# Kernel tuning notes

Hardware: AMD Instinct MI355X
Metric: run time of the kernel (lower is better)

## Reference

```python
import jax, jax.numpy as jnp
import numpy as np

BS, LX, LY, H, MD = 16, 1024, 1024, 512, 512


def setup_inputs() -> dict:
    key = jax.random.key(0)
    ks = jax.random.split(key, 8)
    x = jax.random.normal(ks[0], (BS, LX, H), dtype=jnp.float32)
    y = jax.random.normal(ks[1], (BS, LY, H), dtype=jnp.float32)
    y_mask = jax.random.bernoulli(ks[2], 0.2, (BS, LY))  # True = masked
    s1 = 1.0 / np.sqrt(H)
    W1 = jax.random.uniform(ks[3], (MD, H), jnp.float32, -s1, s1)
    b1 = jax.random.uniform(ks[4], (MD,), jnp.float32, -s1, s1)
    W2 = jax.random.uniform(ks[5], (MD, H), jnp.float32, -s1, s1)
    b2 = jax.random.uniform(ks[6], (MD,), jnp.float32, -s1, s1)
    s2 = 1.0 / np.sqrt(MD)
    k7, k8 = jax.random.split(ks[7])
    w_o = jax.random.uniform(k7, (MD,), jnp.float32, -s2, s2)
    b_o = jax.random.uniform(k8, (), jnp.float32, -s2, s2)
    return {"x": x, "y": y, "y_mask": y_mask, "W1": W1, "b1": b1,
            "W2": W2, "b2": b2, "w_o": w_o, "b_o": b_o}


def reference(x, y, y_mask, W1, b1, W2, b2, w_o, b_o):
    # Projections: [B,L,MD]
    x_proj = jax.nn.relu(jnp.einsum('blh,mh->blm', x, W1) + b1)
    y_proj = jax.nn.relu(jnp.einsum('blh,mh->blm', y, W2) + b2)
    # o_liner is linear, so o_liner(x_i + y_j) = w_o.x_i + w_o.y_j + b_o
    sx = x_proj @ w_o  # [B,Lx]
    sy = y_proj @ w_o  # [B,Ly]
    scores = sx[:, :, None] + sy[:, None, :] + b_o  # [B,Lx,Ly]
    scores = jnp.where(y_mask[:, None, :], jnp.float32(-1e7), scores)
    alpha = jax.nn.softmax(scores, axis=-1)  # softmax over len_y
    return alpha
```

## Files before the change

### kernel.cpp

```cpp
#include <hip/hip_runtime.h>
#include <hip/hip_bf16.h>

#define BS 16
#define LX 1024
#define LY 1024
#define H 512
#define MD 512
#define RY (BS * LY)

typedef __attribute__((ext_vector_type(8))) __bf16 bf16x8;
typedef __attribute__((ext_vector_type(4))) float floatx4;

__device__ __forceinline__ void load_lds16(const __bf16* g, __bf16* l) {
    __builtin_amdgcn_global_load_lds(
        (const __attribute__((address_space(1))) void*)g,
        (__attribute__((address_space(3))) void*)l,
        16, 0, 0);
}

__global__ __launch_bounds__(256) void prep(const float* __restrict__ Y,
                                            const float* __restrict__ W2,
                                            __bf16* __restrict__ yb,
                                            __bf16* __restrict__ wb) {
    const long i = (long)blockIdx.x * 256 + threadIdx.x;
    const float* src; __bf16* dst; long off;
    if (blockIdx.x < 4096) { src = Y;  dst = yb; off = i; }
    else                   { src = W2; dst = wb; off = i - 4096L * 256; }
    const float4 a = *(const float4*)(src + off * 8);
    const float4 b = *(const float4*)(src + off * 8 + 4);
    bf16x8 v = { (__bf16)a.x, (__bf16)a.y, (__bf16)a.z, (__bf16)a.w,
                 (__bf16)b.x, (__bf16)b.y, (__bf16)b.z, (__bf16)b.w };
    *(bf16x8*)(dst + off * 8) = v;
}

#define BM 64
#define BN 128
#define BKT 64
__global__ __launch_bounds__(256) void gemm_sy(const __bf16* __restrict__ yb,
                                               const __bf16* __restrict__ wb,
                                               const float* __restrict__ b2,
                                               const float* __restrict__ wo,
                                               float* __restrict__ part) {
    __shared__ __align__(16) __bf16 As[BM * BKT];
    __shared__ __align__(16) __bf16 Bs[BN * BKT];

    const int tid  = threadIdx.x;
    const int lane = tid & 63;
    const int wave = tid >> 6;
    const int wm = wave >> 1;
    const int wn = wave & 1;
    const int la = lane & 15;
    const int qa = lane >> 4;
    const int nt = blockIdx.x;
    const int mt = blockIdx.y;
    const int m0 = mt * BM, n0 = nt * BN;

    const int lrow = lane >> 3;
    const int lcol = (lane & 7) * 8;

    floatx4 acc[2][4] = {};

    for (int k0 = 0; k0 < H; k0 += BKT) {
        __syncthreads();
        #pragma unroll
        for (int r = 0; r < 2; ++r) {
            const int rb = r * 32 + wave * 8;
            load_lds16(yb + (size_t)(m0 + rb + lrow) * H + k0 + lcol, &As[rb * BKT]);
        }
        #pragma unroll
        for (int r = 0; r < 4; ++r) {
            const int rb = r * 32 + wave * 8;
            load_lds16(wb + (size_t)(n0 + rb + lrow) * H + k0 + lcol, &Bs[rb * BKT]);
        }
        __syncthreads();

        #pragma unroll
        for (int kh = 0; kh < 2; ++kh) {
            bf16x8 afr[2], bfr[4];
            #pragma unroll
            for (int mf = 0; mf < 2; ++mf)
                afr[mf] = *(const bf16x8*)&As[(wm * 32 + mf * 16 + la) * BKT + kh * 32 + qa * 8];
            #pragma unroll
            for (int nf = 0; nf < 4; ++nf)
                bfr[nf] = *(const bf16x8*)&Bs[(wn * 64 + nf * 16 + la) * BKT + kh * 32 + qa * 8];
            #pragma unroll
            for (int mf = 0; mf < 2; ++mf)
                #pragma unroll
                for (int nf = 0; nf < 4; ++nf)
                    acc[mf][nf] = __builtin_amdgcn_mfma_f32_16x16x32_bf16(afr[mf], bfr[nf], acc[mf][nf], 0, 0, 0);
        }
    }

    const int slice = nt * 2 + wn;
    #pragma unroll
    for (int mf = 0; mf < 2; ++mf) {
        #pragma unroll
        for (int reg = 0; reg < 4; ++reg) {
            float s = 0.f;
            #pragma unroll
            for (int nf = 0; nf < 4; ++nf) {
                const int n = n0 + wn * 64 + nf * 16 + la;
                float v = acc[mf][nf][reg] + b2[n];
                v = fmaxf(v, 0.f);
                s += v * wo[n];
            }
            s += __shfl_xor(s, 1);
            s += __shfl_xor(s, 2);
            s += __shfl_xor(s, 4);
            s += __shfl_xor(s, 8);
            if (la == 0) {
                const int m = m0 + wm * 32 + mf * 16 + qa * 4 + reg;
                part[(size_t)slice * RY + m] = s;
            }
        }
    }
}

__global__ __launch_bounds__(256) void softmax_p(const float* __restrict__ part,
                                                 const int* __restrict__ mask,
                                                 float* __restrict__ p) {
    const int b = blockIdx.x;
    const int tid = threadIdx.x;
    __shared__ float red[8];

    float vals[4];
    int   ms[4];
    float mx = -INFINITY;
    #pragma unroll
    for (int c = 0; c < 4; ++c) {
        const int j = c * 256 + tid;
        float v = 0.f;
        #pragma unroll
        for (int t = 0; t < 8; ++t) v += part[t * RY + b * LY + j];
        vals[c] = v;
        ms[c]   = mask[b * LY + j];
        if (!ms[c]) mx = fmaxf(mx, v);
    }
    #pragma unroll
    for (int off = 1; off < 64; off <<= 1) mx = fmaxf(mx, __shfl_xor(mx, off));
    if ((tid & 63) == 0) red[tid >> 6] = mx;
    __syncthreads();
    mx = fmaxf(fmaxf(red[0], red[1]), fmaxf(red[2], red[3]));

    float e[4];
    float sum = 0.f;
    #pragma unroll
    for (int c = 0; c < 4; ++c) {
        e[c] = ms[c] ? 0.f : __expf(vals[c] - mx);
        sum += e[c];
    }
    #pragma unroll
    for (int off = 1; off < 64; off <<= 1) sum += __shfl_xor(sum, off);
    if ((tid & 63) == 0) red[4 + (tid >> 6)] = sum;
    __syncthreads();
    sum = red[4] + red[5] + red[6] + red[7];
    const float inv = 1.0f / sum;

    #pragma unroll
    for (int c = 0; c < 4; ++c)
        p[b * LY + c * 256 + tid] = e[c] * inv;
}

__global__ __launch_bounds__(256) void bcast(const float* __restrict__ p,
                                             float4* __restrict__ out) {
    const int tid = threadIdx.x;
    const long base_row = (long)blockIdx.x * 8;
    const int b = (int)(base_row >> 10);
    const float4 v = *(const float4*)(p + b * LY + tid * 4);
    float4* o = out + base_row * (LY / 4) + tid;
    #pragma unroll
    for (int r = 0; r < 8; ++r) o[r * (LY / 4)] = v;
}

extern "C" void kernel_launch(void* const* d_in, const int* in_sizes, int n_in,
                              void* d_out, int out_size, void* d_ws, size_t ws_size,
                              hipStream_t stream) {
    const float* y  = (const float*)d_in[1];
    const int*   ym = (const int*)  d_in[2];
    const float* W2 = (const float*)d_in[5];
    const float* b2 = (const float*)d_in[6];
    const float* wo = (const float*)d_in[7];

    char* ws = (char*)d_ws;
    __bf16* yb   = (__bf16*)ws;
    __bf16* wb   = (__bf16*)(ws + (size_t)RY * H * 2);
    float*  part = (float*)(ws + (size_t)RY * H * 2 + (size_t)MD * H * 2);
    float*  p    = part + 8 * RY;

    prep<<<4096 + 128, 256, 0, stream>>>(y, W2, yb, wb);
    dim3 gg(MD / BN, RY / BM);
    gemm_sy<<<gg, 256, 0, stream>>>(yb, wb, b2, wo, part);
    softmax_p<<<BS, 256, 0, stream>>>(part, ym, p);
    bcast<<<(BS * LX) / 8, 256, 0, stream>>>(p, (float4*)d_out);
}
```

Baseline: 151.9 us.

## Fuse Y fp32-to-bf16 conversion into GEMM A-tile load with padded LDS

Removes the separate conversion pass over Y and instead loads fp32 Y tiles directly in the GEMM, converting to bf16 in registers before storing to LDS with a padded row stride. The intent is to drop the intermediate bf16 Y write and re-read. In exchange, the GEMM reads fp32 Y (twice the bytes per tile, read by each of four column blocks), and the A path loses the async global-to-LDS load.

```diff
diff --git a/kernel.cpp b/kernel.cpp
--- a/kernel.cpp
+++ b/kernel.cpp
@@ -18,30 +18,26 @@
         16, 0, 0);
 }
 
-__global__ __launch_bounds__(256) void prep(const float* __restrict__ Y,
-                                            const float* __restrict__ W2,
-                                            __bf16* __restrict__ yb,
-                                            __bf16* __restrict__ wb) {
-    const long i = (long)blockIdx.x * 256 + threadIdx.x;
-    const float* src; __bf16* dst; long off;
-    if (blockIdx.x < 4096) { src = Y;  dst = yb; off = i; }
-    else                   { src = W2; dst = wb; off = i - 4096L * 256; }
-    const float4 a = *(const float4*)(src + off * 8);
-    const float4 b = *(const float4*)(src + off * 8 + 4);
+__global__ __launch_bounds__(256) void prep_w2(const float* __restrict__ W2,
+                                               __bf16* __restrict__ wb) {
+    const int i = blockIdx.x * 256 + threadIdx.x;
+    const float4 a = *(const float4*)(W2 + (size_t)i * 8);
+    const float4 b = *(const float4*)(W2 + (size_t)i * 8 + 4);
     bf16x8 v = { (__bf16)a.x, (__bf16)a.y, (__bf16)a.z, (__bf16)a.w,
                  (__bf16)b.x, (__bf16)b.y, (__bf16)b.z, (__bf16)b.w };
-    *(bf16x8*)(dst + off * 8) = v;
+    *(bf16x8*)(wb + (size_t)i * 8) = v;
 }
 
 #define BM 64
 #define BN 128
 #define BKT 64
-__global__ __launch_bounds__(256) void gemm_sy(const __bf16* __restrict__ yb,
+#define ASTR 72
+__global__ __launch_bounds__(256) void gemm_sy(const float* __restrict__ Y,
                                                const __bf16* __restrict__ wb,
                                                const float* __restrict__ b2,
                                                const float* __restrict__ wo,
                                                float* __restrict__ part) {
-    __shared__ __align__(16) __bf16 As[BM * BKT];
+    __shared__ __align__(16) __bf16 As[BM * ASTR];
     __shared__ __align__(16) __bf16 Bs[BN * BKT];
 
     const int tid  = threadIdx.x;
@@ -58,20 +54,29 @@
     const int lrow = lane >> 3;
     const int lcol = (lane & 7) * 8;
 
+    const int ar = tid >> 2;
+    const int ac = (tid & 3) * 16;
+    const float* ybase = Y + (size_t)(m0 + ar) * H + ac;
+
     floatx4 acc[2][4] = {};
 
     for (int k0 = 0; k0 < H; k0 += BKT) {
         __syncthreads();
         #pragma unroll
-        for (int r = 0; r < 2; ++r) {
-            const int rb = r * 32 + wave * 8;
-            load_lds16(yb + (size_t)(m0 + rb + lrow) * H + k0 + lcol, &As[rb * BKT]);
-        }
-        #pragma unroll
         for (int r = 0; r < 4; ++r) {
             const int rb = r * 32 + wave * 8;
             load_lds16(wb + (size_t)(n0 + rb + lrow) * H + k0 + lcol, &Bs[rb * BKT]);
         }
+        const float4 a0 = *(const float4*)(ybase + k0);
+        const float4 a1 = *(const float4*)(ybase + k0 + 4);
+        const float4 a2 = *(const float4*)(ybase + k0 + 8);
+        const float4 a3 = *(const float4*)(ybase + k0 + 12);
+        bf16x8 p0 = { (__bf16)a0.x, (__bf16)a0.y, (__bf16)a0.z, (__bf16)a0.w,
+                      (__bf16)a1.x, (__bf16)a1.y, (__bf16)a1.z, (__bf16)a1.w };
+        bf16x8 p1 = { (__bf16)a2.x, (__bf16)a2.y, (__bf16)a2.z, (__bf16)a2.w,
+                      (__bf16)a3.x, (__bf16)a3.y, (__bf16)a3.z, (__bf16)a3.w };
+        *(bf16x8*)&As[ar * ASTR + ac]     = p0;
+        *(bf16x8*)&As[ar * ASTR + ac + 8] = p1;
         __syncthreads();
 
         #pragma unroll
@@ -79,7 +84,7 @@
             bf16x8 afr[2], bfr[4];
             #pragma unroll
             for (int mf = 0; mf < 2; ++mf)
-                afr[mf] = *(const bf16x8*)&As[(wm * 32 + mf * 16 + la) * BKT + kh * 32 + qa * 8];
+                afr[mf] = *(const bf16x8*)&As[(wm * 32 + mf * 16 + la) * ASTR + kh * 32 + qa * 8];
             #pragma unroll
             for (int nf = 0; nf < 4; ++nf)
                 bfr[nf] = *(const bf16x8*)&Bs[(wn * 64 + nf * 16 + la) * BKT + kh * 32 + qa * 8];
@@ -182,14 +187,13 @@
     const float* wo = (const float*)d_in[7];
 
     char* ws = (char*)d_ws;
-    __bf16* yb   = (__bf16*)ws;
-    __bf16* wb   = (__bf16*)(ws + (size_t)RY * H * 2);
-    float*  part = (float*)(ws + (size_t)RY * H * 2 + (size_t)MD * H * 2);
+    __bf16* wb   = (__bf16*)ws;
+    float*  part = (float*)(ws + (size_t)MD * H * 2);
     float*  p    = part + 8 * RY;
 
-    prep<<<4096 + 128, 256, 0, stream>>>(y, W2, yb, wb);
+    prep_w2<<<(MD * H) / (256 * 8), 256, 0, stream>>>(W2, wb);
     dim3 gg(MD / BN, RY / BM);
-    gemm_sy<<<gg, 256, 0, stream>>>(yb, wb, b2, wo, part);
+    gemm_sy<<<gg, 256, 0, stream>>>(y, wb, b2, wo, part);
     softmax_p<<<BS, 256, 0, stream>>>(part, ym, p);
     bcast<<<(BS * LX) / 8, 256, 0, stream>>>(p, (float4*)d_out);
 }
```

Result: faster. 148.9 us (-2.0%).
